# Kernel tuning notes

Measured on AMD Instinct MI355X. Metric: run time of the kernel, lower is better.

## Reference

```python
import jax, jax.numpy as jnp
import numpy as np

C = 128   # channel_num
S = 56    # spatial size
K = 3     # ksize -> gaussian kernel is 2K x 2K = 6x6


def _gaussian_bank(theta, p, sig, a):
    # Vectorized version of get_gaussian over all (i, u) channel pairs.
    coords = jnp.linspace(-K, K, 2 * K)
    xv, yv = jnp.meshgrid(coords, coords, indexing='ij')  # [2K, 2K]
    ct = jnp.cos(theta)[:, :, None, None]                  # [C, C, 1, 1]
    st = jnp.sin(theta)[:, :, None, None]
    xrot = xv * ct + yv * st                               # [C, C, 2K, 2K]
    yrot = -xv * st + yv * ct
    p2 = (p ** 2)[:, :, None, None]
    s2 = (sig ** 2)[:, :, None, None]
    amp = (a / (2.0 * jnp.pi * p * sig))[:, :, None, None]
    return amp * jnp.exp(-0.5 * (xrot ** 2 / p2 + yrot ** 2 / s2))  # [C, C, 2K, 2K]


def setup_inputs() -> dict:
    key = jax.random.key(0)
    ks = jax.random.split(key, 8)
    scale = 90.0
    theta = scale * jnp.abs(jax.random.normal(ks[0], (C, C)))
    p = scale * jnp.abs(jax.random.normal(ks[1], (C, C))) + 10.0
    sig = scale * jnp.abs(jax.random.normal(ks[2], (C, C))) + 10.0
    a = scale * jnp.abs(jax.random.normal(ks[3], (C, C)))
    nI = jnp.abs(jax.random.normal(ks[4], (C, C)))
    nU = jnp.abs(jax.random.normal(ks[5], (C,)))
    bias = jnp.abs(jax.random.normal(ks[6], (C,)))
    # positive activations (module assumes post-ReLU input; pow of negatives -> NaN)
    x = jax.random.uniform(ks[7], (2, C, S, S), dtype=jnp.float32)
    return {"x": x, "theta": theta, "p": p, "sig": sig, "a": a,
            "nI": nI, "nU": nU, "bias": bias}


def reference(x, theta, p, sig, a, nI, nU, bias):
    B = x.shape[0]
    g = _gaussian_bank(theta, p, sig, a)                     # [C, C, 2K, 2K]
    # x[b,i]^nI[i,u] for all pairs -> [B, C, C, S, S]
    xp = x[:, :, None, :, :] ** nI[None, :, :, None, None]
    xp = xp.reshape(B, C * C, S, S)
    kern = g.reshape(C * C, 1, 2 * K, 2 * K)
    # depthwise cross-correlation per (i,u) pair; even kernel + pad K -> S+1,
    # then crop first row/col (matches output[1:, 1:] in the torch code)
    conv = jax.lax.conv_general_dilated(
        xp, kern, window_strides=(1, 1), padding=((K, K), (K, K)),
        feature_group_count=C * C)                           # [B, C*C, S+1, S+1]
    conv = conv[:, :, 1:, 1:].reshape(B, C, C, S, S)
    denom = (bias ** nU)[None, :, None, None] + conv.sum(axis=2)  # [B, C, S, S]
    num = x ** nU[None, :, None, None]
    return num / denom
```

## Files before the change

kernel.cpp:

```cpp
#include <hip/hip_runtime.h>
#include <math.h>

#define CN 128
#define SN 56
#define PCOLS 33
#define PXPAD 654
#define PXPAD_DW 327
#define DYS (6 * PXPAD + PCOLS)
#define DXS (PXPAD + 1)
#define LOG2E 1.44269504088896341f

typedef float  fr4 __attribute__((ext_vector_type(4)));
typedef short  sh8 __attribute__((ext_vector_type(8)));

__device__ __forceinline__ unsigned short f2bf(float f) {
    unsigned u = __float_as_uint(f);
    u += 0x7FFFu + ((u >> 16) & 1u);
    return (unsigned short)(u >> 16);
}
__device__ __forceinline__ int pk2(float f0, float f1) {
    unsigned u0 = __float_as_uint(f0) + 0x8000u;
    unsigned u1 = __float_as_uint(f1) + 0x8000u;
    return (int)__builtin_amdgcn_perm(u1, u0, 0x07060302u);
}
__device__ __forceinline__ float bf2f(unsigned short s) {
    return __uint_as_float(((unsigned)s) << 16);
}

__global__ void bank_kernel(const float* __restrict__ theta,
                            const float* __restrict__ p,
                            const float* __restrict__ sig,
                            const float* __restrict__ a,
                            unsigned short* __restrict__ bank) {
    int t = blockIdx.x * 256 + threadIdx.x;
    int lane = t & 63;
    int grp  = t >> 6;
    int nt = grp % 3;
    int ks = (grp / 3) & 3;
    int c  = grp / 12;
    int tap = nt * 16 + (lane & 15);
    int ub  = ks * 32 + (lane >> 4) * 8;
    sh8 v = {0,0,0,0,0,0,0,0};
    if (tap < 36) {
        int ky = tap / 6, kx = tap - ky * 6;
        float xv = -3.0f + 1.2f * ky;
        float yv = -3.0f + 1.2f * kx;
        #pragma unroll
        for (int j = 0; j < 8; ++j) {
            int pr = c * CN + ub + j;
            float th = theta[pr], pv = p[pr], sv = sig[pr], av = a[pr];
            float ct = __cosf(th), st = __sinf(th);
            float xr =  xv * ct + yv * st;
            float yr = -xv * st + yv * ct;
            float e  = -0.5f * (xr * xr / (pv * pv) + yr * yr / (sv * sv));
            float g  = (av / (2.0f * 3.14159265358979323846f * pv * sv))
                       * __builtin_amdgcn_exp2f(e * LOG2E);
            v[j] = (short)f2bf(g);
        }
    }
    ((sh8*)bank)[t] = v;
}

__global__ __launch_bounds__(512, 4) void divnorm_mfma(
        const float* __restrict__ x, const unsigned short* __restrict__ bank,
        const float* __restrict__ nI, const float* __restrict__ nU,
        const float* __restrict__ bias, float* __restrict__ out)
{
    __shared__ alignas(16) unsigned short SH[36 * PXPAD];

    const int bid = blockIdx.x;
    const int w   = bid & 1;
    const int h   = (bid >> 1) & 1;
    const int c   = (bid >> 2) & 127;
    const int b   = bid >> 9;
    const int tid = threadIdx.x;
    const int lane = tid & 63;
    const int wv   = tid >> 6;
    const int l15  = lane & 15;
    const int lg   = lane >> 4;

    sh8 Bf[3][4];
    {
        const sh8* bp = (const sh8*)bank + (size_t)c * 768 + lane;
        #pragma unroll
        for (int ks = 0; ks < 4; ++ks)
            #pragma unroll
            for (int nt = 0; nt < 3; ++nt)
                Bf[nt][ks] = bp[(ks * 3 + nt) * 64];
    }

    float nIr[4][8];
    {
        const float* nc = nI + c * CN;
        #pragma unroll
        for (int ks = 0; ks < 4; ++ks) {
            const float4* q = (const float4*)(nc + ks * 32 + lg * 8);
            float4 q0 = q[0], q1 = q[1];
            nIr[ks][0] = q0.x; nIr[ks][1] = q0.y; nIr[ks][2] = q0.z; nIr[ks][3] = q0.w;
            nIr[ks][4] = q1.x; nIr[ks][5] = q1.y; nIr[ks][6] = q1.z; nIr[ks][7] = q1.w;
        }
    }

    const float* xc = x   + (size_t)(b * CN + c) * (SN * SN);
    float*       oc = out + (size_t)(b * CN + c) * (SN * SN);
    const float nUc = nU[c];
    const float bn  = __builtin_amdgcn_exp2f(nUc * __builtin_amdgcn_logf(bias[c]));
    const int   c0m2 = 28 * w - 2;

    const int pof0 = l15 * PXPAD_DW;
    const int pof1 = (16 + l15) * PXPAD_DW;
    const int pof2 = (32 + l15) * PXPAD_DW;

    #pragma unroll 1
    for (int band = 0; band < 2; ++band) {
        const int r0   = 28 * h + 14 * band;
        const int r0m2 = r0 - 2;

        int pidx = wv * 16 + l15;
        int prl  = pidx / PCOLS;
        int pcl  = pidx - prl * PCOLS;
        int prow = r0m2 + prl;
        int pcol = c0m2 + pcl;
        bool val = ((unsigned)prow < 56u) && ((unsigned)pcol < 56u);
        float xv = xc[val ? (prow * SN + pcol) : 0];

        #pragma unroll 1
        for (int i = 0; i < 5; ++i) {
            float L = val ? __builtin_amdgcn_logf(xv) : -1e30f;

            {
                int np   = pidx + 128;
                int nprl = np / PCOLS;
                int npcl = np - nprl * PCOLS;
                int nprw = r0m2 + nprl;
                int npcc = c0m2 + npcl;
                val = ((unsigned)nprw < 56u) && ((unsigned)npcc < 56u);
                xv  = xc[val ? (nprw * SN + npcc) : 0];
                pidx = np;
            }

            fr4 a0 = {0.f,0.f,0.f,0.f}, a1 = {0.f,0.f,0.f,0.f}, a2 = {0.f,0.f,0.f,0.f};
            #pragma unroll
            for (int ks = 0; ks < 4; ++ks) {
                float t[8];
                #pragma unroll
                for (int j = 0; j < 8; ++j)
                    t[j] = __builtin_amdgcn_exp2f(nIr[ks][j] * L);
                int4 ai;
                ai.x = pk2(t[0], t[1]); ai.y = pk2(t[2], t[3]);
                ai.z = pk2(t[4], t[5]); ai.w = pk2(t[6], t[7]);
                sh8 af = *(sh8*)&ai;
                a0 = __builtin_amdgcn_mfma_f32_16x16x32_bf16(af, Bf[0][ks], a0, 0, 0, 0);
                a1 = __builtin_amdgcn_mfma_f32_16x16x32_bf16(af, Bf[1][ks], a1, 0, 0, 0);
                a2 = __builtin_amdgcn_mfma_f32_16x16x32_bf16(af, Bf[2][ks], a2, 0, 0, 0);
            }

            int pbd = (wv + 8 * i) * 8 + lg * 2;
            int* SD = (int*)SH;
            SD[pof0 + pbd]     = pk2(a0[0], a0[1]);
            SD[pof0 + pbd + 1] = pk2(a0[2], a0[3]);
            SD[pof1 + pbd]     = pk2(a1[0], a1[1]);
            SD[pof1 + pbd + 1] = pk2(a1[2], a1[3]);
            if (l15 < 4) {
                SD[pof2 + pbd]     = pk2(a2[0], a2[1]);
                SD[pof2 + pbd + 1] = pk2(a2[2], a2[3]);
            }
        }
        __syncthreads();

        if (tid < 14 * 28) {
            int oy = tid / 28;
            int ox = tid - oy * 28;
            const unsigned short* pb = &SH[oy * PCOLS + ox];
            float s = 0.0f;
            #pragma unroll
            for (int dy = 0; dy < 6; ++dy)
                #pragma unroll
                for (int dx = 0; dx < 6; ++dx)
                    s += bf2f(pb[dy * DYS + dx * DXS]);
            int y  = r0 + oy;
            int xg = c0m2 + 2 + ox;
            float xq  = xc[y * SN + xg];
            float num = __builtin_amdgcn_exp2f(nUc * __builtin_amdgcn_logf(xq));
            oc[y * SN + xg] = num / (bn + s);
        }
        __syncthreads();
    }
}

extern "C" void kernel_launch(void* const* d_in, const int* in_sizes, int n_in,
                              void* d_out, int out_size, void* d_ws, size_t ws_size,
                              hipStream_t stream) {
    const float* x     = (const float*)d_in[0];
    const float* theta = (const float*)d_in[1];
    const float* p     = (const float*)d_in[2];
    const float* sig   = (const float*)d_in[3];
    const float* a     = (const float*)d_in[4];
    const float* nI    = (const float*)d_in[5];
    const float* nU    = (const float*)d_in[6];
    const float* bias  = (const float*)d_in[7];
    float* out = (float*)d_out;
    unsigned short* bank = (unsigned short*)d_ws;

    hipLaunchKernelGGL(bank_kernel, dim3(384), dim3(256), 0, stream,
                       theta, p, sig, a, bank);
    hipLaunchKernelGGL(divnorm_mfma, dim3(2 * CN * 4), dim3(512), 0, stream,
                       x, bank, nI, nU, bias, out);
}
```

Measured before the change: 107.5 us.

## Reuse overlapping halo rows between bands instead of recomputing them

The second row band previously recomputed the powered-input and MFMA convolution tiles for the four halo rows it shares with the first band. After the first band finishes, the shared rows' results are now copied within LDS to the start of the buffer, and the second band computes only the remaining tiles with an uneven per-wave iteration count. This removes about a quarter of the exp and MFMA work in the second band. The cost is an extra LDS copy and barrier, plus some load imbalance across waves. LDS stores are also merged into int2 writes and the plane padding is shrunk, which may change bank-conflict behavior.

Result: no change. 105.6 us (-1.8%).

```diff
diff --git a/kernel.cpp b/kernel.cpp
--- a/kernel.cpp
+++ b/kernel.cpp
@@ -4,10 +4,10 @@
 #define CN 128
 #define SN 56
 #define PCOLS 33
-#define PXPAD 654
-#define PXPAD_DW 327
-#define DYS (6 * PXPAD + PCOLS)
-#define DXS (PXPAD + 1)
+#define SDW 322
+#define PXS 644
+#define DYS (6 * PXS + PCOLS)
+#define DXS (PXS + 1)
 #define LOG2E 1.44269504088896341f
 
 typedef float  fr4 __attribute__((ext_vector_type(4)));
@@ -66,7 +66,8 @@
         const float* __restrict__ nI, const float* __restrict__ nU,
         const float* __restrict__ bias, float* __restrict__ out)
 {
-    __shared__ alignas(16) unsigned short SH[36 * PXPAD];
+    __shared__ alignas(16) unsigned short SH[36 * PXS];
+    int* SD = (int*)SH;
 
     const int bid = blockIdx.x;
     const int w   = bid & 1;
@@ -107,16 +108,18 @@
     const float bn  = __builtin_amdgcn_exp2f(nUc * __builtin_amdgcn_logf(bias[c]));
     const int   c0m2 = 28 * w - 2;
 
-    const int pof0 = l15 * PXPAD_DW;
-    const int pof1 = (16 + l15) * PXPAD_DW;
-    const int pof2 = (32 + l15) * PXPAD_DW;
+    const int pof0 = l15 * SDW;
+    const int pof1 = (16 + l15) * SDW;
+    const int pof2 = (32 + l15) * SDW;
 
     #pragma unroll 1
-    for (int band = 0; band < 2; ++band) {
-        const int r0   = 28 * h + 14 * band;
+    for (int phase = 0; phase < 2; ++phase) {
+        const int r0   = 28 * h + 14 * phase;
         const int r0m2 = r0 - 2;
-
-        int pidx = wv * 16 + l15;
+        const int tb   = phase ? 10 : 0;
+        const int nit  = phase ? ((wv < 6) ? 4 : 3) : 5;
+
+        int pidx = (tb + wv) * 16 + l15;
         int prl  = pidx / PCOLS;
         int pcl  = pidx - prl * PCOLS;
         int prow = r0m2 + prl;
@@ -125,7 +128,7 @@
         float xv = xc[val ? (prow * SN + pcol) : 0];
 
         #pragma unroll 1
-        for (int i = 0; i < 5; ++i) {
+        for (int i = 0; i < nit; ++i) {
             float L = val ? __builtin_amdgcn_logf(xv) : -1e30f;
 
             {
@@ -155,15 +158,16 @@
                 a2 = __builtin_amdgcn_mfma_f32_16x16x32_bf16(af, Bf[2][ks], a2, 0, 0, 0);
             }
 
-            int pbd = (wv + 8 * i) * 8 + lg * 2;
-            int* SD = (int*)SH;
-            SD[pof0 + pbd]     = pk2(a0[0], a0[1]);
-            SD[pof0 + pbd + 1] = pk2(a0[2], a0[3]);
-            SD[pof1 + pbd]     = pk2(a1[0], a1[1]);
-            SD[pof1 + pbd + 1] = pk2(a1[2], a1[3]);
+            int pbd = (tb + wv + 8 * i) * 8 + lg * 2;
+            int2 v0, v1;
+            v0.x = pk2(a0[0], a0[1]); v0.y = pk2(a0[2], a0[3]);
+            v1.x = pk2(a1[0], a1[1]); v1.y = pk2(a1[2], a1[3]);
+            *(int2*)&SD[pof0 + pbd] = v0;
+            *(int2*)&SD[pof1 + pbd] = v1;
             if (l15 < 4) {
-                SD[pof2 + pbd]     = pk2(a2[0], a2[1]);
-                SD[pof2 + pbd + 1] = pk2(a2[2], a2[3]);
+                int2 v2;
+                v2.x = pk2(a2[0], a2[1]); v2.y = pk2(a2[2], a2[3]);
+                *(int2*)&SD[pof2 + pbd] = v2;
             }
         }
         __syncthreads();
@@ -185,6 +189,15 @@
             oc[y * SN + xg] = num / (bn + s);
         }
         __syncthreads();
+
+        if (phase == 0) {
+            for (int idx = tid; idx < 36 * 80; idx += 512) {
+                int pl  = idx / 80;
+                int off = idx - pl * 80;
+                SD[pl * SDW + off] = SD[pl * SDW + 231 + off];
+            }
+            __syncthreads();
+        }
     }
 }
 
```
